# Optimization experiments

Measured on AMD Instinct MI355X. Metric: run time of the kernel, lower is better.

Reference implementation:

```python
import jax, jax.numpy as jnp
import numpy as np

ITEMS_TOTAL = 50000
DIM = 64
BATCH = 16
N_PER_GRAPH = 50


def setup_inputs() -> dict:
    key = jax.random.key(0)
    k1, k2, k3, k4 = jax.random.split(key, 4)
    nodes = jax.random.randint(k1, (BATCH * N_PER_GRAPH,), 0, ITEMS_TOTAL, dtype=jnp.int64)
    nodes_output = jax.random.normal(k2, (BATCH * N_PER_GRAPH, DIM), dtype=jnp.float32)
    emb_table = jax.random.normal(k3, (ITEMS_TOTAL, DIM), dtype=jnp.float32)
    alpha = jax.random.uniform(k4, (ITEMS_TOTAL, 1), dtype=jnp.float32)  # torch.rand init
    return {"nodes": nodes, "nodes_output": nodes_output, "emb_table": emb_table,
            "alpha": alpha, "n_per_graph": N_PER_GRAPH}


def reference(nodes, nodes_output, emb_table, alpha, n_per_graph):
    items_total, dim = emb_table.shape
    n = int(n_per_graph)
    b = nodes.shape[0] // n
    idx_b = nodes.reshape(b, n)            # (B, n) item indices per graph
    feat_b = nodes_output.reshape(b, n, dim)  # (B, n, F)

    def per_graph(idx, feat):
        # beta: 1 for items present in this graph, 0 otherwise
        beta = jnp.zeros((items_total, 1), dtype=emb_table.dtype).at[idx].set(1.0)
        # gate the full table: untouched rows keep emb, touched rows scaled by (1-alpha)
        embed = (1.0 - beta * alpha) * emb_table          # (items_total, F)
        updated = embed[idx] + alpha[idx] * feat          # (n, F)
        return embed.at[idx].set(updated)

    return jax.vmap(per_graph)(idx_b, feat_b)             # (B, items_total, F)
```

## Files before the change

### kernel.cpp

```cpp
#include <hip/hip_runtime.h>


#define DIM 64
#define SEGS (DIM / 4)
#define BLOCK 256
#define KF 5
#define TILE (BLOCK * KF)
#define NROWS (TILE / SEGS)

template <int CB>
__global__ __launch_bounds__(BLOCK) void ggu_bcast(
    const int* __restrict__ nodes,
    const float4* __restrict__ feat,
    const float4* __restrict__ emb,
    const float* __restrict__ alpha,
    float4* __restrict__ out,
    int items, int n, int Brt)
{
    const int B = (CB > 0) ? CB : Brt;
    const size_t rowsF4 = (size_t)items * SEGS;
    const size_t base   = (size_t)blockIdx.x * TILE;
    const int row0      = (int)(base / SEGS);
    const int tid       = threadIdx.x;

    extern __shared__ int smem[];
    int* lastj = smem;
    unsigned* tmaskp = (unsigned*)(smem + B * NROWS);

    for (int t = tid; t < B * NROWS; t += BLOCK) lastj[t] = -1;
    if (tid == 0) *tmaskp = 0u;
    __syncthreads();
    const int total = B * n;
    for (int t = tid; t < total; t += BLOCK) {
        const int local = nodes[t] - row0;
        if ((unsigned)local < (unsigned)NROWS) {
            const int b = t / n;
            atomicMax(&lastj[b * NROWS + local], t);
            atomicOr(tmaskp, 1u << b);
        }
    }
    __syncthreads();
    const unsigned tm = *tmaskp;

    float4 v[KF];
    const float4* e = emb + base;
    #pragma unroll
    for (int k = 0; k < KF; ++k) {
        const size_t off = (size_t)(k * BLOCK + tid);
        v[k] = (base + off < rowsF4) ? e[off] : float4{0, 0, 0, 0};
    }

    for (int b = 0; b < B; ++b) {
        float4* ob = out + (size_t)b * rowsF4 + base;
        if (!((tm >> b) & 1u)) {
            #pragma unroll
            for (int k = 0; k < KF; ++k) {
                const size_t off = (size_t)(k * BLOCK + tid);
                if (base + off < rowsF4) ob[off] = v[k];
            }
        } else {
            #pragma unroll
            for (int k = 0; k < KF; ++k) {
                const size_t off = (size_t)(k * BLOCK + tid);
                if (base + off >= rowsF4) continue;
                float4 t4 = v[k];
                const int ioff = k * BLOCK + tid;
                const int jl = lastj[b * NROWS + (ioff >> 4)];
                if (jl >= 0) {
                    const int row = row0 + (ioff >> 4);
                    const float a = alpha[row];
                    const float4 f = feat[(size_t)jl * SEGS + (ioff & (SEGS - 1))];
                    const float om = 1.0f - a;
                    t4.x = om * t4.x + a * f.x;
                    t4.y = om * t4.y + a * f.y;
                    t4.z = om * t4.z + a * f.z;
                    t4.w = om * t4.w + a * f.w;
                }
                ob[off] = t4;
            }
        }
    }
}

extern "C" void kernel_launch(void* const* d_in, const int* in_sizes, int n_in,
                              void* d_out, int out_size, void* d_ws, size_t ws_size,
                              hipStream_t stream) {
    const int*   nodes = (const int*)d_in[0];
    const float* feat  = (const float*)d_in[1];
    const float* emb   = (const float*)d_in[2];
    const float* alpha = (const float*)d_in[3];

    const int items = in_sizes[3];
    const int B     = out_size / (items * DIM);
    const int n     = in_sizes[0] / B;

    const size_t rowsF4 = (size_t)items * SEGS;
    const unsigned grid = (unsigned)((rowsF4 + TILE - 1) / TILE);
    const size_t lds_bytes = (size_t)(B * NROWS + 1) * sizeof(int);

    if (B == 16) {
        ggu_bcast<16><<<grid, BLOCK, lds_bytes, stream>>>(
            nodes, (const float4*)feat, (const float4*)emb, alpha,
            (float4*)d_out, items, n, B);
    } else {
        ggu_bcast<0><<<grid, BLOCK, lds_bytes, stream>>>(
            nodes, (const float4*)feat, (const float4*)emb, alpha,
            (float4*)d_out, items, n, B);
    }
}
```

Before: 220.3 us.

## Use nontemporal loads/stores, stagger batch order per block, shrink tile

Replaces the regular global loads and stores of the embedding table and output with nontemporal builtins, so the roughly 205 MB output write stream does not pollute the caches. The batch loop now starts at a different graph per block, spreading concurrent writes across separate output regions. The tile shrinks from 5 to 2 float4 per thread, which raises the block count at the cost of each block rescanning the node list more often.

```diff
diff --git a/kernel.cpp b/kernel.cpp
--- a/kernel.cpp
+++ b/kernel.cpp
@@ -4,17 +4,19 @@
 #define DIM 64
 #define SEGS (DIM / 4)
 #define BLOCK 256
-#define KF 5
+#define KF 2
 #define TILE (BLOCK * KF)
 #define NROWS (TILE / SEGS)
 
+typedef float vf4 __attribute__((ext_vector_type(4)));
+
 template <int CB>
-__global__ __launch_bounds__(BLOCK) void ggu_bcast(
+__global__ __launch_bounds__(BLOCK) void ggu_nt(
     const int* __restrict__ nodes,
     const float4* __restrict__ feat,
-    const float4* __restrict__ emb,
+    const vf4* __restrict__ emb,
     const float* __restrict__ alpha,
-    float4* __restrict__ out,
+    vf4* __restrict__ out,
     int items, int n, int Brt)
 {
     const int B = (CB > 0) ? CB : Brt;
@@ -42,28 +44,37 @@
     __syncthreads();
     const unsigned tm = *tmaskp;
 
-    float4 v[KF];
-    const float4* e = emb + base;
+    vf4 v[KF];
+    const vf4* e = emb + base;
     #pragma unroll
     for (int k = 0; k < KF; ++k) {
         const size_t off = (size_t)(k * BLOCK + tid);
-        v[k] = (base + off < rowsF4) ? e[off] : float4{0, 0, 0, 0};
+        v[k] = (base + off < rowsF4) ? __builtin_nontemporal_load(e + off)
+                                     : (vf4){0.0f, 0.0f, 0.0f, 0.0f};
     }
 
-    for (int b = 0; b < B; ++b) {
-        float4* ob = out + (size_t)b * rowsF4 + base;
+    for (int bb = 0; bb < B; ++bb) {
+        int b;
+        if (CB == 16) {
+            b = (blockIdx.x + bb) & 15;
+        } else {
+            b = (int)(blockIdx.x % B) + bb;
+            if (b >= B) b -= B;
+        }
+        vf4* ob = out + (size_t)b * rowsF4 + base;
         if (!((tm >> b) & 1u)) {
             #pragma unroll
             for (int k = 0; k < KF; ++k) {
                 const size_t off = (size_t)(k * BLOCK + tid);
-                if (base + off < rowsF4) ob[off] = v[k];
+                if (base + off < rowsF4)
+                    __builtin_nontemporal_store(v[k], ob + off);
             }
         } else {
             #pragma unroll
             for (int k = 0; k < KF; ++k) {
                 const size_t off = (size_t)(k * BLOCK + tid);
                 if (base + off >= rowsF4) continue;
-                float4 t4 = v[k];
+                vf4 t4 = v[k];
                 const int ioff = k * BLOCK + tid;
                 const int jl = lastj[b * NROWS + (ioff >> 4)];
                 if (jl >= 0) {
@@ -76,7 +87,7 @@
                     t4.z = om * t4.z + a * f.z;
                     t4.w = om * t4.w + a * f.w;
                 }
-                ob[off] = t4;
+                __builtin_nontemporal_store(t4, ob + off);
             }
         }
     }
@@ -99,12 +110,12 @@
     const size_t lds_bytes = (size_t)(B * NROWS + 1) * sizeof(int);
 
     if (B == 16) {
-        ggu_bcast<16><<<grid, BLOCK, lds_bytes, stream>>>(
-            nodes, (const float4*)feat, (const float4*)emb, alpha,
-            (float4*)d_out, items, n, B);
+        ggu_nt<16><<<grid, BLOCK, lds_bytes, stream>>>(
+            nodes, (const float4*)feat, (const vf4*)emb, alpha,
+            (vf4*)d_out, items, n, B);
     } else {
-        ggu_bcast<0><<<grid, BLOCK, lds_bytes, stream>>>(
-            nodes, (const float4*)feat, (const float4*)emb, alpha,
-            (float4*)d_out, items, n, B);
+        ggu_nt<0><<<grid, BLOCK, lds_bytes, stream>>>(
+            nodes, (const float4*)feat, (const vf4*)emb, alpha,
+            (vf4*)d_out, items, n, B);
     }
 }
```

Measured after the change: 225.6 us. 1.02x slower.
